# Optimization experiments

Hardware: AMD Instinct MI355X
Metric: run time of the kernel (lower is better)

Reference implementation:

```python
import jax, jax.numpy as jnp
import numpy as np

N = 20000   # nodes
E = 320000  # edges per adjacency (avg degree 16)
D = 256     # feature dim


def setup_inputs() -> dict:
    key = jax.random.key(0)
    ks = jax.random.split(key, 7)
    x = jax.random.normal(ks[0], (N, D), dtype=jnp.float32)
    row1 = jax.random.randint(ks[1], (E,), 0, N, dtype=jnp.int32)
    col1 = jax.random.randint(ks[2], (E,), 0, N, dtype=jnp.int32)
    val1 = jax.random.uniform(ks[3], (E,), dtype=jnp.float32)
    row2 = jax.random.randint(ks[4], (E,), 0, N, dtype=jnp.int32)
    col2 = jax.random.randint(ks[5], (E,), 0, N, dtype=jnp.int32)
    val2 = jax.random.uniform(ks[6], (E,), dtype=jnp.float32)
    return {"x": x, "row1": row1, "col1": col1, "val1": val1,
            "row2": row2, "col2": col2, "val2": val2}


def _spmm(row, col, val, x, num_segments):
    # out[i] = sum_{e: row[e]==i} val[e] * x[col[e]]  (COO SpMM)
    msgs = val[:, None] * x[col]           # [E, D] gathered+weighted messages
    return jax.ops.segment_sum(msgs, row, num_segments=num_segments)


def reference(x, row1, col1, val1, row2, col2, val2):
    n = x.shape[0]
    x1 = _spmm(row1, col1, val1, x, n)     # matmul(adj_t, x)
    x2 = _spmm(row2, col2, val2, x, n)     # matmul(adj_t2, x)
    return jnp.concatenate([x1, x2], axis=1)  # [N, 2D]
```

## Files before the change

### kernel.cpp

```cpp
#include <hip/hip_runtime.h>


#define NODES 20000
#define D_FEAT 256
#define OUT_STRIDE (2 * D_FEAT)
#define NR (2 * NODES)
#define CAP 64
#define SPILL_CAP 4096

typedef float vfloat4 __attribute__((ext_vector_type(4)));
typedef int   vint2   __attribute__((ext_vector_type(2)));
typedef unsigned short vushort8 __attribute__((ext_vector_type(8)));

__device__ __forceinline__ unsigned short f2bf(float f) {
    unsigned u = __float_as_uint(f);
    unsigned r = u + 0x7FFFu + ((u >> 16) & 1u);
    return (unsigned short)(r >> 16);
}
__device__ __forceinline__ float bf2f(unsigned short h) {
    return __uint_as_float((unsigned)h << 16);
}


__global__ __launch_bounds__(256) void k1_build(
    const int* __restrict__ row1, const int* __restrict__ col1,
    const float* __restrict__ val1, int E1,
    const int* __restrict__ row2, const int* __restrict__ col2,
    const float* __restrict__ val2, int E2,
    int* __restrict__ cnt, int* __restrict__ spill_cnt,
    int4* __restrict__ spill, int2* __restrict__ pairs,
    const float* __restrict__ x, unsigned short* __restrict__ xh,
    int edge_blocks, int conv_elems)
{
    if ((int)blockIdx.x < edge_blocks) {
        const int i = blockIdx.x * 256 + threadIdx.x;
        const int Et = E1 + E2;
        if (i >= Et) return;
        int rj, c; float v;
        if (i < E1) { rj = row1[i];                 c = col1[i]; v = val1[i]; }
        else { const int e = i - E1; rj = NODES + row2[e]; c = col2[e]; v = val2[e]; }
        const int rank = atomicAdd(&cnt[rj], 1);
        if (rank < CAP) {
            pairs[(size_t)rj * CAP + rank] = make_int2(c, __float_as_int(v));
        } else {
            const int s = atomicAdd(spill_cnt, 1);
            if (s < SPILL_CAP)
                spill[s] = make_int4(rj, c, __float_as_int(v), 0);
        }
    } else {
        const int b = blockIdx.x - edge_blocks;
        const long base = ((long)b * 256 + threadIdx.x) * 8;
        if (base >= conv_elems) return;
        const float4 a = reinterpret_cast<const float4*>(x + base)[0];
        const float4 c = reinterpret_cast<const float4*>(x + base)[1];
        vushort8 h;
        h.s0 = f2bf(a.x); h.s1 = f2bf(a.y); h.s2 = f2bf(a.z); h.s3 = f2bf(a.w);
        h.s4 = f2bf(c.x); h.s5 = f2bf(c.y); h.s6 = f2bf(c.z); h.s7 = f2bf(c.w);
        *reinterpret_cast<vushort8*>(xh + base) = h;
    }
}


__global__ __launch_bounds__(256) void k4_spmm(
    const unsigned short* __restrict__ xh, float* __restrict__ out,
    const int* __restrict__ cnt, const int2* __restrict__ pairs,
    const int* __restrict__ spill_cnt, const int4* __restrict__ spill)
{
    const int wid  = threadIdx.x >> 6;
    const int lane = threadIdx.x & 63;
    const int r = blockIdx.x * 4 + wid;
    if (r >= NODES) return;
    const int half = blockIdx.y;
    const int rj = half * NODES + r;

    const int deg = min(cnt[rj], CAP);
    int c = 0; float v = 0.f;
    if (lane < deg) {
        const vint2 p = __builtin_nontemporal_load(
            reinterpret_cast<const vint2*>(pairs) + (size_t)rj * CAP + lane);
        c = p.x; v = __int_as_float(p.y);
    }

    float4 acc = {0.f, 0.f, 0.f, 0.f};
    int k = 0;
    for (; k + 4 <= deg; k += 4) {
        const int   c0 = __shfl(c, k + 0), c1 = __shfl(c, k + 1);
        const int   c2 = __shfl(c, k + 2), c3 = __shfl(c, k + 3);
        const float v0 = __shfl(v, k + 0), v1 = __shfl(v, k + 1);
        const float v2 = __shfl(v, k + 2), v3 = __shfl(v, k + 3);
        const ushort4 h0 = reinterpret_cast<const ushort4*>(xh + (size_t)c0 * D_FEAT)[lane];
        const ushort4 h1 = reinterpret_cast<const ushort4*>(xh + (size_t)c1 * D_FEAT)[lane];
        const ushort4 h2 = reinterpret_cast<const ushort4*>(xh + (size_t)c2 * D_FEAT)[lane];
        const ushort4 h3 = reinterpret_cast<const ushort4*>(xh + (size_t)c3 * D_FEAT)[lane];
        acc.x += v0 * bf2f(h0.x); acc.y += v0 * bf2f(h0.y);
        acc.z += v0 * bf2f(h0.z); acc.w += v0 * bf2f(h0.w);
        acc.x += v1 * bf2f(h1.x); acc.y += v1 * bf2f(h1.y);
        acc.z += v1 * bf2f(h1.z); acc.w += v1 * bf2f(h1.w);
        acc.x += v2 * bf2f(h2.x); acc.y += v2 * bf2f(h2.y);
        acc.z += v2 * bf2f(h2.z); acc.w += v2 * bf2f(h2.w);
        acc.x += v3 * bf2f(h3.x); acc.y += v3 * bf2f(h3.y);
        acc.z += v3 * bf2f(h3.z); acc.w += v3 * bf2f(h3.w);
    }
    for (; k < deg; ++k) {
        const int   ck = __shfl(c, k);
        const float vk = __shfl(v, k);
        const ushort4 h = reinterpret_cast<const ushort4*>(xh + (size_t)ck * D_FEAT)[lane];
        acc.x += vk * bf2f(h.x); acc.y += vk * bf2f(h.y);
        acc.z += vk * bf2f(h.z); acc.w += vk * bf2f(h.w);
    }

    const int sc = min(*spill_cnt, SPILL_CAP);
    for (int s = 0; s < sc; ++s) {
        const int4 sp = spill[s];
        if (sp.x == rj) {
            const float sv = __int_as_float(sp.z);
            const ushort4 h = reinterpret_cast<const ushort4*>(xh + (size_t)sp.y * D_FEAT)[lane];
            acc.x += sv * bf2f(h.x); acc.y += sv * bf2f(h.y);
            acc.z += sv * bf2f(h.z); acc.w += sv * bf2f(h.w);
        }
    }

    vfloat4 accv; accv.x = acc.x; accv.y = acc.y; accv.z = acc.z; accv.w = acc.w;
    vfloat4* dst = reinterpret_cast<vfloat4*>(
        out + (size_t)r * OUT_STRIDE + half * D_FEAT) + lane;
    __builtin_nontemporal_store(accv, dst);
}


__global__ __launch_bounds__(256) void spmm_edge_atomic(
    const int* __restrict__ row, const int* __restrict__ col,
    const float* __restrict__ val, const float* __restrict__ x,
    float* __restrict__ out, int num_edges, int col_off)
{
    const int wave_in_block = threadIdx.x >> 6;
    const int lane = threadIdx.x & 63;
    const int e = blockIdx.x * 4 + wave_in_block;
    if (e >= num_edges) return;
    const int r = row[e];
    const int c = col[e];
    const float v = val[e];
    const float4 xv = reinterpret_cast<const float4*>(x + (size_t)c * D_FEAT)[lane];
    float* orow = out + (size_t)r * OUT_STRIDE + col_off + lane * 4;
    atomicAdd(orow + 0, v * xv.x);
    atomicAdd(orow + 1, v * xv.y);
    atomicAdd(orow + 2, v * xv.z);
    atomicAdd(orow + 3, v * xv.w);
}

extern "C" void kernel_launch(void* const* d_in, const int* in_sizes, int n_in,
                              void* d_out, int out_size, void* d_ws, size_t ws_size,
                              hipStream_t stream)
{
    const float* x    = (const float*)d_in[0];
    const int*   row1 = (const int*)d_in[1];
    const int*   col1 = (const int*)d_in[2];
    const float* val1 = (const float*)d_in[3];
    const int*   row2 = (const int*)d_in[4];
    const int*   col2 = (const int*)d_in[5];
    const float* val2 = (const float*)d_in[6];
    float* out = (float*)d_out;

    const int E1 = in_sizes[1];
    const int E2 = in_sizes[4];
    const int Et = E1 + E2;
    const int conv_elems = NODES * D_FEAT;

    const size_t o_cnt   = 0;
    const size_t o_scnt  = o_cnt + NR;
    const size_t o_spill = (o_scnt + 1 + 3) & ~(size_t)3;
    const size_t o_pairs = o_spill + 4 * (size_t)SPILL_CAP;
    const size_t o_xh    = o_pairs + 2 * (size_t)NR * CAP;
    const size_t need_ints = o_xh + (size_t)conv_elems / 2;

    if (ws_size < need_ints * sizeof(int) || (o_pairs & 1) || (o_xh & 3)) {
        (void)hipMemsetAsync(d_out, 0, (size_t)out_size * sizeof(float), stream);
        spmm_edge_atomic<<<dim3((E1 + 3) / 4), 256, 0, stream>>>(
            row1, col1, val1, x, out, E1, 0);
        spmm_edge_atomic<<<dim3((E2 + 3) / 4), 256, 0, stream>>>(
            row2, col2, val2, x, out, E2, D_FEAT);
        return;
    }

    int* w = (int*)d_ws;
    int*  cnt       = w + o_cnt;
    int*  spill_cnt = w + o_scnt;
    int4* spill     = (int4*)(w + o_spill);
    int2* pairs     = (int2*)(w + o_pairs);
    unsigned short* xh = (unsigned short*)(w + o_xh);

    (void)hipMemsetAsync(cnt, 0, (o_spill - o_cnt) * sizeof(int), stream);

    const int edge_blocks = (Et + 255) / 256;
    const int conv_blocks = (conv_elems + 256 * 8 - 1) / (256 * 8);
    k1_build<<<dim3(edge_blocks + conv_blocks), 256, 0, stream>>>(
        row1, col1, val1, E1, row2, col2, val2, E2,
        cnt, spill_cnt, spill, pairs, x, xh, edge_blocks, conv_elems);
    k4_spmm<<<dim3((NODES + 3) / 4, 2), 256, 0, stream>>>(
        xh, out, cnt, pairs, spill_cnt, spill);
}
```

Before: 163.5 us.

## Replicate per-row bucket counters eightfold and compact neighbours via ballot into LDS

The edge bucketing now spreads each row's atomic counter and slot storage across 8 replicas, chosen by block index, each holding up to 8 edges. The aim is to reduce atomic contention on hot rows. The SpMM kernel reads all 8 replica counts per row, compacts the valid entries with a ballot/popcount prefix into a per-wave LDS buffer, and reads neighbour indices from LDS instead of using shuffles. In exchange, the counter memset grows eightfold, each row needs more scattered counter loads, and the spill capacity is enlarged because a replica overflows at only 8 edges.

```diff
diff --git a/kernel.cpp b/kernel.cpp
--- a/kernel.cpp
+++ b/kernel.cpp
@@ -5,8 +5,9 @@
 #define D_FEAT 256
 #define OUT_STRIDE (2 * D_FEAT)
 #define NR (2 * NODES)
-#define CAP 64
-#define SPILL_CAP 4096
+#define REP 8
+#define CAP_R 8
+#define SPILL_CAP 16384
 
 typedef float vfloat4 __attribute__((ext_vector_type(4)));
 typedef int   vint2   __attribute__((ext_vector_type(2)));
@@ -27,7 +28,8 @@
     const float* __restrict__ val1, int E1,
     const int* __restrict__ row2, const int* __restrict__ col2,
     const float* __restrict__ val2, int E2,
-    int* __restrict__ cnt, int* __restrict__ spill_cnt,
+    int* __restrict__ cnt,
+    int* __restrict__ spill_cnt,
     int4* __restrict__ spill, int2* __restrict__ pairs,
     const float* __restrict__ x, unsigned short* __restrict__ xh,
     int edge_blocks, int conv_elems)
@@ -39,9 +41,11 @@
         int rj, c; float v;
         if (i < E1) { rj = row1[i];                 c = col1[i]; v = val1[i]; }
         else { const int e = i - E1; rj = NODES + row2[e]; c = col2[e]; v = val2[e]; }
-        const int rank = atomicAdd(&cnt[rj], 1);
-        if (rank < CAP) {
-            pairs[(size_t)rj * CAP + rank] = make_int2(c, __float_as_int(v));
+        const int rep = blockIdx.x & (REP - 1);
+        const int rank = atomicAdd(&cnt[(size_t)rep * NR + rj], 1);
+        if (rank < CAP_R) {
+            pairs[((size_t)rj * REP + rep) * CAP_R + rank] =
+                make_int2(c, __float_as_int(v));
         } else {
             const int s = atomicAdd(spill_cnt, 1);
             if (s < SPILL_CAP)
@@ -66,6 +70,7 @@
     const int* __restrict__ cnt, const int2* __restrict__ pairs,
     const int* __restrict__ spill_cnt, const int4* __restrict__ spill)
 {
+    __shared__ int2 lbuf[4][64];
     const int wid  = threadIdx.x >> 6;
     const int lane = threadIdx.x & 63;
     const int r = blockIdx.x * 4 + wid;
@@ -73,25 +78,33 @@
     const int half = blockIdx.y;
     const int rj = half * NODES + r;
 
-    const int deg = min(cnt[rj], CAP);
-    int c = 0; float v = 0.f;
-    if (lane < deg) {
+    const int rep  = lane >> 3;
+    const int slot = lane & 7;
+    const int dr = min(cnt[(size_t)rep * NR + rj], CAP_R);
+    const bool valid = slot < dr;
+    const unsigned long long mask = __ballot(valid);
+    const int deg = __popcll(mask);
+    const int pos = __popcll(mask & ((1ull << lane) - 1ull));
+    if (valid) {
         const vint2 p = __builtin_nontemporal_load(
-            reinterpret_cast<const vint2*>(pairs) + (size_t)rj * CAP + lane);
-        c = p.x; v = __int_as_float(p.y);
+            reinterpret_cast<const vint2*>(pairs) +
+            ((size_t)rj * REP + rep) * CAP_R + slot);
+        lbuf[wid][pos] = make_int2(p.x, p.y);
     }
 
     float4 acc = {0.f, 0.f, 0.f, 0.f};
     int k = 0;
     for (; k + 4 <= deg; k += 4) {
-        const int   c0 = __shfl(c, k + 0), c1 = __shfl(c, k + 1);
-        const int   c2 = __shfl(c, k + 2), c3 = __shfl(c, k + 3);
-        const float v0 = __shfl(v, k + 0), v1 = __shfl(v, k + 1);
-        const float v2 = __shfl(v, k + 2), v3 = __shfl(v, k + 3);
-        const ushort4 h0 = reinterpret_cast<const ushort4*>(xh + (size_t)c0 * D_FEAT)[lane];
-        const ushort4 h1 = reinterpret_cast<const ushort4*>(xh + (size_t)c1 * D_FEAT)[lane];
-        const ushort4 h2 = reinterpret_cast<const ushort4*>(xh + (size_t)c2 * D_FEAT)[lane];
-        const ushort4 h3 = reinterpret_cast<const ushort4*>(xh + (size_t)c3 * D_FEAT)[lane];
+        const int2 p0 = lbuf[wid][k + 0];
+        const int2 p1 = lbuf[wid][k + 1];
+        const int2 p2 = lbuf[wid][k + 2];
+        const int2 p3 = lbuf[wid][k + 3];
+        const float v0 = __int_as_float(p0.y), v1 = __int_as_float(p1.y);
+        const float v2 = __int_as_float(p2.y), v3 = __int_as_float(p3.y);
+        const ushort4 h0 = reinterpret_cast<const ushort4*>(xh + (size_t)p0.x * D_FEAT)[lane];
+        const ushort4 h1 = reinterpret_cast<const ushort4*>(xh + (size_t)p1.x * D_FEAT)[lane];
+        const ushort4 h2 = reinterpret_cast<const ushort4*>(xh + (size_t)p2.x * D_FEAT)[lane];
+        const ushort4 h3 = reinterpret_cast<const ushort4*>(xh + (size_t)p3.x * D_FEAT)[lane];
         acc.x += v0 * bf2f(h0.x); acc.y += v0 * bf2f(h0.y);
         acc.z += v0 * bf2f(h0.z); acc.w += v0 * bf2f(h0.w);
         acc.x += v1 * bf2f(h1.x); acc.y += v1 * bf2f(h1.y);
@@ -102,9 +115,9 @@
         acc.z += v3 * bf2f(h3.z); acc.w += v3 * bf2f(h3.w);
     }
     for (; k < deg; ++k) {
-        const int   ck = __shfl(c, k);
-        const float vk = __shfl(v, k);
-        const ushort4 h = reinterpret_cast<const ushort4*>(xh + (size_t)ck * D_FEAT)[lane];
+        const int2 p = lbuf[wid][k];
+        const float vk = __int_as_float(p.y);
+        const ushort4 h = reinterpret_cast<const ushort4*>(xh + (size_t)p.x * D_FEAT)[lane];
         acc.x += vk * bf2f(h.x); acc.y += vk * bf2f(h.y);
         acc.z += vk * bf2f(h.z); acc.w += vk * bf2f(h.w);
     }
@@ -166,10 +179,10 @@
     const int conv_elems = NODES * D_FEAT;
 
     const size_t o_cnt   = 0;
-    const size_t o_scnt  = o_cnt + NR;
+    const size_t o_scnt  = o_cnt + (size_t)REP * NR;
     const size_t o_spill = (o_scnt + 1 + 3) & ~(size_t)3;
     const size_t o_pairs = o_spill + 4 * (size_t)SPILL_CAP;
-    const size_t o_xh    = o_pairs + 2 * (size_t)NR * CAP;
+    const size_t o_xh    = o_pairs + 2 * (size_t)NR * REP * CAP_R;
     const size_t need_ints = o_xh + (size_t)conv_elems / 2;
 
     if (ws_size < need_ints * sizeof(int) || (o_pairs & 1) || (o_xh & 3)) {
```

Measured after the change: 176.1 us. +7.7%, slower.

## Split CSR build into replicated count, prefix, and place passes

Applied to the files above, without the earlier changes.

The single build kernel, which did atomic slot allocation and a scattered pair write in one pass, becomes three kernels. The count pass increments one of eight replicated counters chosen by block index and records each edge's local rank; a small pass turns the replicated counts into per-replica bases and a clamped degree; a place pass writes each edge's pair at base plus rank. The intent is to spread contention on the per-row atomic counters. In exchange it adds two kernel launches, re-reads the edge arrays, adds the rank array traffic, and enlarges the spill buffer.

```diff
diff --git a/kernel.cpp b/kernel.cpp
--- a/kernel.cpp
+++ b/kernel.cpp
@@ -5,8 +5,9 @@
 #define D_FEAT 256
 #define OUT_STRIDE (2 * D_FEAT)
 #define NR (2 * NODES)
+#define REP 8
 #define CAP 64
-#define SPILL_CAP 4096
+#define SPILL_CAP 16384
 
 typedef float vfloat4 __attribute__((ext_vector_type(4)));
 typedef int   vint2   __attribute__((ext_vector_type(2)));
@@ -22,13 +23,11 @@
 }
 
 
-__global__ __launch_bounds__(256) void k1_build(
-    const int* __restrict__ row1, const int* __restrict__ col1,
-    const float* __restrict__ val1, int E1,
-    const int* __restrict__ row2, const int* __restrict__ col2,
-    const float* __restrict__ val2, int E2,
-    int* __restrict__ cnt, int* __restrict__ spill_cnt,
-    int4* __restrict__ spill, int2* __restrict__ pairs,
+__global__ __launch_bounds__(256) void k1a_count(
+    const int* __restrict__ row1, int E1,
+    const int* __restrict__ row2, int E2,
+    int* __restrict__ cnt,
+    unsigned short* __restrict__ rankl,
     const float* __restrict__ x, unsigned short* __restrict__ xh,
     int edge_blocks, int conv_elems)
 {
@@ -36,17 +35,9 @@
         const int i = blockIdx.x * 256 + threadIdx.x;
         const int Et = E1 + E2;
         if (i >= Et) return;
-        int rj, c; float v;
-        if (i < E1) { rj = row1[i];                 c = col1[i]; v = val1[i]; }
-        else { const int e = i - E1; rj = NODES + row2[e]; c = col2[e]; v = val2[e]; }
-        const int rank = atomicAdd(&cnt[rj], 1);
-        if (rank < CAP) {
-            pairs[(size_t)rj * CAP + rank] = make_int2(c, __float_as_int(v));
-        } else {
-            const int s = atomicAdd(spill_cnt, 1);
-            if (s < SPILL_CAP)
-                spill[s] = make_int4(rj, c, __float_as_int(v), 0);
-        }
+        const int rj = (i < E1) ? row1[i] : (NODES + row2[i - E1]);
+        const int rep = blockIdx.x & (REP - 1);
+        rankl[i] = (unsigned short)atomicAdd(&cnt[(size_t)rep * NR + rj], 1);
     } else {
         const int b = blockIdx.x - edge_blocks;
         const long base = ((long)b * 256 + threadIdx.x) * 8;
@@ -61,9 +52,53 @@
 }
 
 
+__global__ __launch_bounds__(256) void k1b_bases(
+    int* __restrict__ cnt, int* __restrict__ deg)
+{
+    const int row = blockIdx.x * 256 + threadIdx.x;
+    if (row >= NR) return;
+    int run = 0;
+    #pragma unroll
+    for (int r = 0; r < REP; ++r) {
+        const int c = cnt[(size_t)r * NR + row];
+        cnt[(size_t)r * NR + row] = run;
+        run += c;
+    }
+    deg[row] = min(run, CAP);
+}
+
+
+__global__ __launch_bounds__(256) void k1c_place(
+    const int* __restrict__ row1, const int* __restrict__ col1,
+    const float* __restrict__ val1, int E1,
+    const int* __restrict__ row2, const int* __restrict__ col2,
+    const float* __restrict__ val2, int E2,
+    const int* __restrict__ cnt,
+    const unsigned short* __restrict__ rankl,
+    int2* __restrict__ pairs,
+    int* __restrict__ spill_cnt, int4* __restrict__ spill)
+{
+    const int i = blockIdx.x * 256 + threadIdx.x;
+    const int Et = E1 + E2;
+    if (i >= Et) return;
+    int rj, c; float v;
+    if (i < E1) { rj = row1[i];                 c = col1[i]; v = val1[i]; }
+    else { const int e = i - E1; rj = NODES + row2[e]; c = col2[e]; v = val2[e]; }
+    const int rep = blockIdx.x & (REP - 1);
+    const int pos = cnt[(size_t)rep * NR + rj] + (int)rankl[i];
+    if (pos < CAP) {
+        pairs[(size_t)rj * CAP + pos] = make_int2(c, __float_as_int(v));
+    } else {
+        const int s = atomicAdd(spill_cnt, 1);
+        if (s < SPILL_CAP)
+            spill[s] = make_int4(rj, c, __float_as_int(v), 0);
+    }
+}
+
+
 __global__ __launch_bounds__(256) void k4_spmm(
     const unsigned short* __restrict__ xh, float* __restrict__ out,
-    const int* __restrict__ cnt, const int2* __restrict__ pairs,
+    const int* __restrict__ deg, const int2* __restrict__ pairs,
     const int* __restrict__ spill_cnt, const int4* __restrict__ spill)
 {
     const int wid  = threadIdx.x >> 6;
@@ -73,9 +108,9 @@
     const int half = blockIdx.y;
     const int rj = half * NODES + r;
 
-    const int deg = min(cnt[rj], CAP);
+    const int dg = deg[rj];
     int c = 0; float v = 0.f;
-    if (lane < deg) {
+    if (lane < dg) {
         const vint2 p = __builtin_nontemporal_load(
             reinterpret_cast<const vint2*>(pairs) + (size_t)rj * CAP + lane);
         c = p.x; v = __int_as_float(p.y);
@@ -83,7 +118,7 @@
 
     float4 acc = {0.f, 0.f, 0.f, 0.f};
     int k = 0;
-    for (; k + 4 <= deg; k += 4) {
+    for (; k + 4 <= dg; k += 4) {
         const int   c0 = __shfl(c, k + 0), c1 = __shfl(c, k + 1);
         const int   c2 = __shfl(c, k + 2), c3 = __shfl(c, k + 3);
         const float v0 = __shfl(v, k + 0), v1 = __shfl(v, k + 1);
@@ -101,7 +136,7 @@
         acc.x += v3 * bf2f(h3.x); acc.y += v3 * bf2f(h3.y);
         acc.z += v3 * bf2f(h3.z); acc.w += v3 * bf2f(h3.w);
     }
-    for (; k < deg; ++k) {
+    for (; k < dg; ++k) {
         const int   ck = __shfl(c, k);
         const float vk = __shfl(v, k);
         const ushort4 h = reinterpret_cast<const ushort4*>(xh + (size_t)ck * D_FEAT)[lane];
@@ -166,10 +201,12 @@
     const int conv_elems = NODES * D_FEAT;
 
     const size_t o_cnt   = 0;
-    const size_t o_scnt  = o_cnt + NR;
-    const size_t o_spill = (o_scnt + 1 + 3) & ~(size_t)3;
+    const size_t o_scnt  = o_cnt + (size_t)REP * NR;
+    const size_t o_deg   = o_scnt + 4;
+    const size_t o_rank  = o_deg + NR;
+    const size_t o_spill = (o_rank + ((size_t)Et + 1) / 2 + 3) & ~(size_t)3;
     const size_t o_pairs = o_spill + 4 * (size_t)SPILL_CAP;
-    const size_t o_xh    = o_pairs + 2 * (size_t)NR * CAP;
+    const size_t o_xh    = (o_pairs + 2 * (size_t)NR * CAP + 3) & ~(size_t)3;
     const size_t need_ints = o_xh + (size_t)conv_elems / 2;
 
     if (ws_size < need_ints * sizeof(int) || (o_pairs & 1) || (o_xh & 3)) {
@@ -184,17 +221,22 @@
     int* w = (int*)d_ws;
     int*  cnt       = w + o_cnt;
     int*  spill_cnt = w + o_scnt;
+    int*  deg       = w + o_deg;
+    unsigned short* rankl = (unsigned short*)(w + o_rank);
     int4* spill     = (int4*)(w + o_spill);
     int2* pairs     = (int2*)(w + o_pairs);
     unsigned short* xh = (unsigned short*)(w + o_xh);
 
-    (void)hipMemsetAsync(cnt, 0, (o_spill - o_cnt) * sizeof(int), stream);
+    (void)hipMemsetAsync(cnt, 0, (o_deg - o_cnt) * sizeof(int), stream);
 
     const int edge_blocks = (Et + 255) / 256;
     const int conv_blocks = (conv_elems + 256 * 8 - 1) / (256 * 8);
-    k1_build<<<dim3(edge_blocks + conv_blocks), 256, 0, stream>>>(
+    k1a_count<<<dim3(edge_blocks + conv_blocks), 256, 0, stream>>>(
+        row1, E1, row2, E2, cnt, rankl, x, xh, edge_blocks, conv_elems);
+    k1b_bases<<<dim3((NR + 255) / 256), 256, 0, stream>>>(cnt, deg);
+    k1c_place<<<dim3(edge_blocks), 256, 0, stream>>>(
         row1, col1, val1, E1, row2, col2, val2, E2,
-        cnt, spill_cnt, spill, pairs, x, xh, edge_blocks, conv_elems);
+        cnt, rankl, pairs, spill_cnt, spill);
     k4_spmm<<<dim3((NODES + 3) / 4, 2), 256, 0, stream>>>(
-        xh, out, cnt, pairs, spill_cnt, spill);
-}
+        xh, out, deg, pairs, spill_cnt, spill);
+}
```

Measured after the change: 168.4 us. 1.03x slower.
